# Kernel tuning notes

Hardware: AMD Instinct MI355X
Metric: run time of the kernel (lower is better)

## Reference

```python
import jax, jax.numpy as jnp
import numpy as np

NEG_INF = -1e30


def setup_inputs() -> dict:
    key = jax.random.key(0)
    kx, km, kq, kk, kv, ko = jax.random.split(key, 6)
    B, D, L = 2, 1024, 2048
    H, DK = 16, 64
    x = jax.random.normal(kx, (B, D, L), dtype=jnp.float32)
    mask = (jax.random.uniform(km, (B, L)) < 0.9).astype(jnp.float32)
    # per-head projection weights, stacked: (H, D, DK); output proj (D, H*DK)==(D, D)
    sq = 1.0 / np.sqrt(D)
    Wq = jax.random.normal(kq, (H, D, DK), dtype=jnp.float32) * sq
    Wk = jax.random.normal(kk, (H, D, DK), dtype=jnp.float32) * sq
    Wv = jax.random.normal(kv, (H, D, DK), dtype=jnp.float32) * sq
    Wo = jax.random.normal(ko, (D, H * DK), dtype=jnp.float32) * sq
    return {"x": x, "mask": mask, "Wq": Wq, "Wk": Wk, "Wv": Wv, "Wo": Wo}


def reference(x, mask, Wq, Wk, Wv, Wo):
    # x: (B, D, L); original transposes to (B, L, D)
    B, D, L = x.shape
    H, _, DK = Wq.shape
    xt = jnp.transpose(x, (0, 2, 1))  # (B, L, D)
    q = jnp.einsum('bld,hdk->bhlk', xt, Wq)
    k = jnp.einsum('bld,hdk->bhlk', xt, Wk)
    v = jnp.einsum('bld,hdk->bhlk', xt, Wv)
    scores = jnp.einsum('bhlk,bhmk->bhlm', q, k) * (1.0 / np.sqrt(DK))
    # masked log-softmax over keys (hmask), squad-style: mask*logit + (1-mask)*-1e30
    hmask = mask[:, None, None, :]  # (B,1,1,Lk)
    masked = hmask * scores + (1.0 - hmask) * NEG_INF
    logp = jax.nn.log_softmax(masked, axis=-1)
    # second softmax over the log-probs, then multiplicative vmask on query dim
    p = jax.nn.softmax(logp, axis=-1) * mask[:, None, :, None]
    heads = jnp.einsum('bhlm,bhmk->bhlk', p, v)  # (B,H,L,DK)
    head = jnp.transpose(heads, (0, 2, 1, 3)).reshape(B, L, H * DK)
    out = jnp.einsum('ble,de->bld', head, Wo)  # matmul(head, Wo) with Wo (D, H*DK)... 
    # NOTE: torch.matmul(head, Wo) treats Wo as (H*DK_in, D_out) only if square; here
    # Wo is (D, H*DK) with D == H*DK, and torch contracts head's last dim with Wo's FIRST dim:
    out = head @ Wo  # (B, L, H*DK) @ (D, H*DK) requires D==H*DK; contracts dim 0 of Wo
    return jnp.transpose(out, (0, 2, 1))  # (B, D, L)


if __name__ == "__main__":
    print(reference(**setup_inputs()).shape)
```

## Files before the change

### kernel.cpp

```cpp
#include <hip/hip_runtime.h>
#include <hip/hip_bf16.h>

typedef unsigned short u16;
typedef unsigned int u32;
typedef unsigned long long u64;
typedef short s8v __attribute__((ext_vector_type(8)));
typedef short s4v __attribute__((ext_vector_type(4)));
typedef __bf16 bfv8 __attribute__((ext_vector_type(8)));
typedef float f4 __attribute__((ext_vector_type(4)));

static constexpr int B = 2, D = 1024, L = 2048, H = 16, DK = 64, E = 1024;
static constexpr float QSCALE = 0.125f * 1.44269504088896340736f;
static constexpr float SMB = -16.0f;
static constexpr float MASKB = -12000.0f;

#define DEV __device__ __forceinline__

DEV u16 f2bf(float f) {
  unsigned int u = __float_as_uint(f);
  u += 0x7FFFu + ((u >> 16) & 1u);
  return (u16)(u >> 16);
}
DEV float fexp2(float x) { return __builtin_amdgcn_exp2f(x); }
DEV u32 pkbf(float a, float b) {
  __hip_bfloat162 h = __float22bfloat162_rn(float2{a, b});
  u32 r;
  __builtin_memcpy(&r, &h, 4);
  return r;
}
DEV bfv8 cat8(s4v a, s4v b) {
  s8v r;
#pragma unroll
  for (int i = 0; i < 4; ++i) {
    r[i] = a[i];
    r[i + 4] = b[i];
  }
  return __builtin_bit_cast(bfv8, r);
}
DEV int kperm(int kk) {
  return (kk & 96) | (((kk >> 2) & 3) << 3) | (((kk >> 4) & 1) << 2) |
         (kk & 3);
}

#define GLD_LDS16(gp, lp)                                                     \
  __builtin_amdgcn_global_load_lds(                                           \
      (const __attribute__((address_space(1))) void*)(gp),                    \
      (__attribute__((address_space(3))) void*)(lp), 16, 0, 0)

__global__ __launch_bounds__(256) void k_prep(
    const float* __restrict__ x, const float* __restrict__ Wq,
    const float* __restrict__ Wk, const float* __restrict__ Wv,
    const float* __restrict__ Wo, u16* __restrict__ xt, u16* __restrict__ Wt,
    u16* __restrict__ WoT) {
  __shared__ u16 t[64][67];
  const int tid = threadIdx.x;
  const int g = blockIdx.x;
  const float* src;
  u16* dst;
  int sld, dld;
  if (g < 1024) {
    const int b = g >> 9, dt = (g >> 5) & 15, lt = g & 31;
    src = x + ((size_t)b * D + dt * 64) * L + lt * 64;
    sld = L;
    dst = xt + ((size_t)b * L + lt * 64) * D + dt * 64;
    dld = D;
  } else if (g < 1792) {
    const int u = g - 1024;
    const int w = u >> 8, h = (u >> 4) & 15, dt = u & 15;
    const float* Ws = (w == 0) ? Wq : ((w == 1) ? Wk : Wv);
    src = Ws + ((size_t)h * D + dt * 64) * DK;
    sld = DK;
    dst = Wt + ((size_t)(w * H + h) * DK) * D + dt * 64;
    dld = D;
  } else {
    const int v = g - 1792;
    const int et = v >> 4, dt = v & 15;
    src = Wo + ((size_t)et * 64) * D + dt * 64;
    sld = D;
    dst = WoT + ((size_t)dt * 64) * E + et * 64;
    dld = E;
  }
  const int r = tid >> 2, c16 = (tid & 3) * 16;
#pragma unroll
  for (int j = 0; j < 16; j += 4) {
    const f4 v4 = *(const f4*)(src + (size_t)r * sld + c16 + j);
    t[r][c16 + j]     = f2bf(v4[0]);
    t[r][c16 + j + 1] = f2bf(v4[1]);
    t[r][c16 + j + 2] = f2bf(v4[2]);
    t[r][c16 + j + 3] = f2bf(v4[3]);
  }
  __syncthreads();
  s8v o0, o1;
#pragma unroll
  for (int i = 0; i < 8; ++i) {
    o0[i] = (short)t[c16 + i][r];
    o1[i] = (short)t[c16 + 8 + i][r];
  }
  *(s8v*)(dst + (size_t)r * dld + c16)     = o0;
  *(s8v*)(dst + (size_t)r * dld + c16 + 8) = o1;
}

template <int AR>
DEV void gemm_tile(const u16* __restrict__ A, const u16* __restrict__ Bt,
                   int arow0, int brow0, u16* As, u16* Bs,
                   f4 (&acc)[AR / 32][4]) {
  const int tid = threadIdx.x;
  const int wid = tid >> 6, lane = tid & 63;
  const int q = lane >> 4, ln = lane & 15;
  const int wr = wid >> 1, wc = wid & 1;
  const int lrow = lane >> 3;
  const int lc = (lane & 7) ^ lrow;
  const int f0 = (q ^ (ln & 7)) * 8;
  const int f1 = ((q + 4) ^ (ln & 7)) * 8;
  constexpr int MT = AR / 32;

  for (int k0 = 0; k0 < 1024; k0 += 64) {
    __syncthreads();
#pragma unroll
    for (int j = 0; j < AR / 32; ++j) {
      const int rb = wid * (AR / 4) + j * 8;
      GLD_LDS16(A + (size_t)(arow0 + rb + lrow) * 1024 + k0 + lc * 8,
                As + rb * 64);
    }
#pragma unroll
    for (int j = 0; j < 4; ++j) {
      const int rb = wid * 32 + j * 8;
      GLD_LDS16(Bt + (size_t)(brow0 + rb + lrow) * 1024 + k0 + lc * 8,
                Bs + rb * 64);
    }
    __syncthreads();
#pragma unroll
    for (int ks = 0; ks < 2; ++ks) {
      const int fc = ks ? f1 : f0;
      bfv8 af[MT], bf[4];
#pragma unroll
      for (int mt = 0; mt < MT; ++mt)
        af[mt] = *(const bfv8*)(As + (wr * (AR / 2) + mt * 16 + ln) * 64 + fc);
#pragma unroll
      for (int nt = 0; nt < 4; ++nt)
        bf[nt] = *(const bfv8*)(Bs + (wc * 64 + nt * 16 + ln) * 64 + fc);
#pragma unroll
      for (int mt = 0; mt < MT; ++mt)
#pragma unroll
        for (int nt = 0; nt < 4; ++nt)
          acc[mt][nt] = __builtin_amdgcn_mfma_f32_16x16x32_bf16(
              af[mt], bf[nt], acc[mt][nt], 0, 0, 0);
    }
  }
}

__global__ __launch_bounds__(256, 3) void k_qkvg(
    const u16* __restrict__ xt, const u16* __restrict__ Wt,
    u16* __restrict__ Q, u16* __restrict__ K, u16* __restrict__ Vt) {
  __shared__ u16 As[128 * 64];
  __shared__ u16 Bs[128 * 64];
  const int bm = blockIdx.x, bn = blockIdx.y;
  f4 acc[4][4];
#pragma unroll
  for (int mt = 0; mt < 4; ++mt)
#pragma unroll
    for (int nt = 0; nt < 4; ++nt) acc[mt][nt] = (f4){0.f, 0.f, 0.f, 0.f};
  gemm_tile<128>(xt, Wt, bm * 128, bn * 128, As, Bs, acc);

  const int tid = threadIdx.x, wid = tid >> 6, lane = tid & 63;
  const int q = lane >> 4, ln = lane & 15;
  const int wr = wid >> 1, wc = wid & 1;
  const int h2 = bn * 2 + wc;
  const int wsel = h2 >> 4, h = h2 & 15;
  const int b = bm >> 4;
  const int lbase = (bm & 15) * 128 + wr * 64;
  if (wsel == 0) {
    u16* dst = Q + (size_t)(b * H + h) * L * DK;
#pragma unroll
    for (int mt = 0; mt < 4; ++mt)
#pragma unroll
      for (int nt = 0; nt < 4; ++nt)
#pragma unroll
        for (int r = 0; r < 4; ++r)
          dst[(size_t)(lbase + mt * 16 + q * 4 + r) * DK + nt * 16 + ln] =
              f2bf(acc[mt][nt][r] * QSCALE);
  } else if (wsel == 1) {
    u16* dst = K + (size_t)(b * H + h) * L * DK;
#pragma unroll
    for (int mt = 0; mt < 4; ++mt)
#pragma unroll
      for (int nt = 0; nt < 4; ++nt)
#pragma unroll
        for (int r = 0; r < 4; ++r)
          dst[(size_t)(lbase + mt * 16 + q * 4 + r) * DK + nt * 16 + ln] =
              f2bf(acc[mt][nt][r]);
  } else {
    u16* dst = Vt + (size_t)(b * H + h) * DK * L;
#pragma unroll
    for (int mt = 0; mt < 4; ++mt)
#pragma unroll
      for (int nt = 0; nt < 4; ++nt) {
        const u64 pk = (u64)pkbf(acc[mt][nt][0], acc[mt][nt][1]) |
                       ((u64)pkbf(acc[mt][nt][2], acc[mt][nt][3]) << 32);
        *(u64*)(dst + (size_t)(nt * 16 + ln) * L + lbase + mt * 16 + q * 4) =
            pk;
      }
  }
}

__global__ __launch_bounds__(512, 4) void k_attn(
    const u16* __restrict__ Q, const u16* __restrict__ K,
    const u16* __restrict__ Vt, const float* __restrict__ mask,
    u16* __restrict__ Hd) {
  __shared__ u16 kt[2][128 * 64];
  __shared__ u16 vt[2][2][64 * 64];
  __shared__ __align__(16) float mb[L];
  const int h = blockIdx.x, lt = blockIdx.y, b = blockIdx.z;
  const int tid = threadIdx.x;
  const int w = tid >> 6, lane = tid & 63, q = lane >> 4, ln = lane & 15;
  const int wq = w >> 1, wk = w & 1;
  for (int i = tid; i < L; i += 512)
    mb[i] = (mask[(size_t)b * L + i] != 0.0f) ? SMB : MASKB;

  const int bh = b * H + h;
  const u16* Qp = Q + (size_t)bh * L * DK;
  const u16* Kp = K + (size_t)bh * L * DK;
  const u16* Vp = Vt + (size_t)bh * DK * L;
  const int lq = lt * 128 + wq * 32;

  bfv8 qf[2][2];
#pragma unroll
  for (int mt = 0; mt < 2; ++mt) {
    qf[mt][0] = *(const bfv8*)(Qp + (size_t)(lq + mt * 16 + ln) * DK + q * 8);
    qf[mt][1] =
        *(const bfv8*)(Qp + (size_t)(lq + mt * 16 + ln) * DK + 32 + q * 8);
  }

  const int lrow = lane >> 3;
  const int lc = (lane & 7) ^ lrow;
  const int c0 = (q ^ (ln & 7)) * 8;
  const int c1 = ((q + 4) ^ (ln & 7)) * 8;
  int kpr[2];
#pragma unroll
  for (int j = 0; j < 2; ++j) kpr[j] = kperm(w * 16 + j * 8 + lrow);

  auto stage = [&](int m0, int bufi) {
#pragma unroll
    for (int j = 0; j < 2; ++j) {
      GLD_LDS16(Kp + (size_t)(m0 + kpr[j]) * DK + lc * 8,
                &kt[bufi][(w * 16 + j * 8) * 64]);
    }
    const int fr = w * 8 + lrow;
#pragma unroll
    for (int kh = 0; kh < 2; ++kh) {
      GLD_LDS16(Vp + (size_t)fr * L + m0 + kh * 64 + lc * 8,
                &vt[bufi][kh][(w * 8) * 64]);
    }
  };

  union {
    f4 v;
    float f[4];
  } ot[2][4];
#pragma unroll
  for (int mt = 0; mt < 2; ++mt)
#pragma unroll
    for (int dt = 0; dt < 4; ++dt) ot[mt][dt].v = (f4){0.f, 0.f, 0.f, 0.f};
  float lp[2] = {0.f, 0.f};

  stage(0, 0);
  for (int it = 0; it < L / 128; ++it) {
    const int m0 = it * 128;
    __syncthreads();
    if (it + 1 < L / 128) stage(m0 + 128, (it + 1) & 1);
    const int cur = it & 1;
    const u16* ktc = &kt[cur][0];
    const u16* vtc = &vt[cur][wk][0];

    s4v pbe[2];
    bfv8 pbx[2][2];
#pragma unroll
    for (int nt = 0; nt < 4; ++nt) {
      const int krow = wk * 64 + nt * 16 + ln;
      const bfv8 kf0 = *(const bfv8*)(ktc + krow * 64 + c0);
      const bfv8 kf1 = *(const bfv8*)(ktc + krow * 64 + c1);
      const f4 mbv = *(const f4*)(mb + m0 + wk * 64 + (nt >> 1) * 32 +
                                  (nt & 1) * 4 + q * 8);
#pragma unroll
      for (int mt = 0; mt < 2; ++mt) {
        f4 a = mbv;
        __builtin_amdgcn_s_setprio(1);
        a = __builtin_amdgcn_mfma_f32_16x16x32_bf16(kf0, qf[mt][0], a, 0, 0,
                                                    0);
        a = __builtin_amdgcn_mfma_f32_16x16x32_bf16(kf1, qf[mt][1], a, 0, 0,
                                                    0);
        __builtin_amdgcn_s_setprio(0);
        const float p0 = fexp2(a[0]);
        const float p1 = fexp2(a[1]);
        const float p2 = fexp2(a[2]);
        const float p3 = fexp2(a[3]);
        lp[mt] += (p0 + p1) + (p2 + p3);
        const u64 pk = (u64)pkbf(p0, p1) | ((u64)pkbf(p2, p3) << 32);
        const s4v pc = __builtin_bit_cast(s4v, pk);
        if (nt & 1)
          pbx[mt][nt >> 1] = cat8(pbe[mt], pc);
        else
          pbe[mt] = pc;
      }
    }
    __builtin_amdgcn_s_setprio(1);
#pragma unroll
    for (int g = 0; g < 2; ++g) {
#pragma unroll
      for (int dt = 0; dt < 4; ++dt) {
        const int vrow = dt * 16 + ln;
        const bfv8 av =
            *(const bfv8*)(vtc + vrow * 64 + (((g * 4 + q) ^ (ln & 7)) * 8));
#pragma unroll
        for (int mt = 0; mt < 2; ++mt)
          ot[mt][dt].v = __builtin_amdgcn_mfma_f32_16x16x32_bf16(
              av, pbx[mt][g], ot[mt][dt].v, 0, 0, 0);
      }
    }
    __builtin_amdgcn_s_setprio(0);
  }
#pragma unroll
  for (int mt = 0; mt < 2; ++mt) {
    lp[mt] += __shfl_xor(lp[mt], 16);
    lp[mt] += __shfl_xor(lp[mt], 32);
  }
  __syncthreads();
  float* sOt = (float*)&kt[0][0];
  float* sLp = (float*)&vt[0][0][0];
  if (wk) {
#pragma unroll
    for (int mt = 0; mt < 2; ++mt) {
#pragma unroll
      for (int dt = 0; dt < 4; ++dt)
        *(f4*)(sOt + ((((wq * 2 + mt) * 4 + dt) * 64) + lane) * 4) =
            ot[mt][dt].v;
      sLp[(wq * 2 + mt) * 64 + lane] = lp[mt];
    }
  }
  __syncthreads();
  if (!wk) {
#pragma unroll
    for (int mt = 0; mt < 2; ++mt) {
#pragma unroll
      for (int dt = 0; dt < 4; ++dt)
        ot[mt][dt].v +=
            *(const f4*)(sOt + ((((wq * 2 + mt) * 4 + dt) * 64) + lane) * 4);
      lp[mt] += sLp[(wq * 2 + mt) * 64 + lane];
      const float linv =
          (mb[lq + mt * 16 + ln] > -100.0f) ? (1.0f / lp[mt]) : 0.0f;
#pragma unroll
      for (int dt = 0; dt < 4; ++dt) {
        const u64 pk =
            (u64)pkbf(ot[mt][dt].f[0] * linv, ot[mt][dt].f[1] * linv) |
            ((u64)pkbf(ot[mt][dt].f[2] * linv, ot[mt][dt].f[3] * linv) << 32);
        *(u64*)(Hd + (size_t)(b * L + lq + mt * 16 + ln) * E + h * DK +
                dt * 16 + q * 4) = pk;
      }
    }
  }
}

__global__ __launch_bounds__(256, 2) void k_projg(const u16* __restrict__ WoT,
                                                  const u16* __restrict__ Hd,
                                                  float* __restrict__ out) {
  __shared__ u16 As[64 * 64];
  __shared__ u16 Bs[128 * 64];
  const int bm = blockIdx.x, bn = blockIdx.y;
  f4 acc[2][4];
#pragma unroll
  for (int mt = 0; mt < 2; ++mt)
#pragma unroll
    for (int nt = 0; nt < 4; ++nt) acc[mt][nt] = (f4){0.f, 0.f, 0.f, 0.f};
  gemm_tile<64>(WoT, Hd, bm * 64, bn * 128, As, Bs, acc);

  const int tid = threadIdx.x, wid = tid >> 6, lane = tid & 63;
  const int q = lane >> 4, ln = lane & 15;
  const int wr = wid >> 1, wc = wid & 1;
#pragma unroll
  for (int mt = 0; mt < 2; ++mt)
#pragma unroll
    for (int nt = 0; nt < 4; ++nt)
#pragma unroll
      for (int r = 0; r < 4; ++r) {
        const int d = bm * 64 + wr * 32 + mt * 16 + q * 4 + r;
        const int n = bn * 128 + wc * 64 + nt * 16 + ln;
        const int bb = n >> 11, l = n & 2047;
        out[((size_t)(bb * D + d)) * L + l] = acc[mt][nt][r];
      }
}

extern "C" void kernel_launch(void* const* d_in, const int* in_sizes, int n_in,
                              void* d_out, int out_size, void* d_ws,
                              size_t ws_size, hipStream_t stream) {
  const float* x    = (const float*)d_in[0];
  const float* mask = (const float*)d_in[1];
  const float* Wq   = (const float*)d_in[2];
  const float* Wk   = (const float*)d_in[3];
  const float* Wv   = (const float*)d_in[4];
  const float* Wo   = (const float*)d_in[5];
  u16* ws = (u16*)d_ws;
  u16* Qws  = ws;
  u16* Kws  = ws + 4194304;
  u16* Vtws = ws + 8388608;
  u16* WoTw = ws + 12582912;
  u16* Wtws = ws + 13631488;
  u16* xtws = ws + 16777216;
  u16* Hdws = ws + 16777216;

  k_prep<<<2048, 256, 0, stream>>>(x, Wq, Wk, Wv, Wo, xtws, Wtws, WoTw);
  k_qkvg<<<dim3(32, 24), 256, 0, stream>>>(xtws, Wtws, Qws, Kws, Vtws);
  k_attn<<<dim3(16, 16, 2), 512, 0, stream>>>(Qws, Kws, Vtws, mask, Hdws);
  k_projg<<<dim3(16, 32), 256, 0, stream>>>(WoTw, Hdws, (float*)d_out);
}
```

Baseline: 174.0 us.

## Remap block indices per XCD for L2 locality and shrink projection tiles

All three GEMM/attention launches become 1D grids. Block IDs are remapped so that blocks scheduled on the same XCD (round-robin by blockIdx mod 8) share A/B tiles or the same batch-head, which should improve per-XCD L2 reuse. The output projection also moves to 64x64 tiles with a higher occupancy bound, giving 1024 blocks instead of 512. Smaller tiles lower arithmetic intensity per block and add redundant operand loads.

```diff
diff --git a/kernel.cpp b/kernel.cpp
--- a/kernel.cpp
+++ b/kernel.cpp
@@ -100,10 +100,10 @@
   *(s8v*)(dst + (size_t)r * dld + c16 + 8) = o1;
 }
 
-template <int AR>
+template <int AR, int BR>
 DEV void gemm_tile(const u16* __restrict__ A, const u16* __restrict__ Bt,
                    int arow0, int brow0, u16* As, u16* Bs,
-                   f4 (&acc)[AR / 32][4]) {
+                   f4 (&acc)[AR / 32][BR / 32]) {
   const int tid = threadIdx.x;
   const int wid = tid >> 6, lane = tid & 63;
   const int q = lane >> 4, ln = lane & 15;
@@ -112,7 +112,7 @@
   const int lc = (lane & 7) ^ lrow;
   const int f0 = (q ^ (ln & 7)) * 8;
   const int f1 = ((q + 4) ^ (ln & 7)) * 8;
-  constexpr int MT = AR / 32;
+  constexpr int MT = AR / 32, NT = BR / 32;
 
   for (int k0 = 0; k0 < 1024; k0 += 64) {
     __syncthreads();
@@ -123,8 +123,8 @@
                 As + rb * 64);
     }
 #pragma unroll
-    for (int j = 0; j < 4; ++j) {
-      const int rb = wid * 32 + j * 8;
+    for (int j = 0; j < BR / 32; ++j) {
+      const int rb = wid * (BR / 4) + j * 8;
       GLD_LDS16(Bt + (size_t)(brow0 + rb + lrow) * 1024 + k0 + lc * 8,
                 Bs + rb * 64);
     }
@@ -132,17 +132,17 @@
 #pragma unroll
     for (int ks = 0; ks < 2; ++ks) {
       const int fc = ks ? f1 : f0;
-      bfv8 af[MT], bf[4];
+      bfv8 af[MT], bf[NT];
 #pragma unroll
       for (int mt = 0; mt < MT; ++mt)
         af[mt] = *(const bfv8*)(As + (wr * (AR / 2) + mt * 16 + ln) * 64 + fc);
 #pragma unroll
-      for (int nt = 0; nt < 4; ++nt)
-        bf[nt] = *(const bfv8*)(Bs + (wc * 64 + nt * 16 + ln) * 64 + fc);
+      for (int nt = 0; nt < NT; ++nt)
+        bf[nt] = *(const bfv8*)(Bs + (wc * (BR / 2) + nt * 16 + ln) * 64 + fc);
 #pragma unroll
       for (int mt = 0; mt < MT; ++mt)
 #pragma unroll
-        for (int nt = 0; nt < 4; ++nt)
+        for (int nt = 0; nt < NT; ++nt)
           acc[mt][nt] = __builtin_amdgcn_mfma_f32_16x16x32_bf16(
               af[mt], bf[nt], acc[mt][nt], 0, 0, 0);
     }
@@ -154,13 +154,16 @@
     u16* __restrict__ Q, u16* __restrict__ K, u16* __restrict__ Vt) {
   __shared__ u16 As[128 * 64];
   __shared__ u16 Bs[128 * 64];
-  const int bm = blockIdx.x, bn = blockIdx.y;
+  const int orig = blockIdx.x;
+  const int xcd = orig & 7, kk = orig >> 3;
+  const int bm = (xcd >> 1) * 8 + (kk & 7);
+  const int bn = (xcd & 1) * 12 + (kk >> 3);
   f4 acc[4][4];
 #pragma unroll
   for (int mt = 0; mt < 4; ++mt)
 #pragma unroll
     for (int nt = 0; nt < 4; ++nt) acc[mt][nt] = (f4){0.f, 0.f, 0.f, 0.f};
-  gemm_tile<128>(xt, Wt, bm * 128, bn * 128, As, Bs, acc);
+  gemm_tile<128, 128>(xt, Wt, bm * 128, bn * 128, As, Bs, acc);
 
   const int tid = threadIdx.x, wid = tid >> 6, lane = tid & 63;
   const int q = lane >> 4, ln = lane & 15;
@@ -210,14 +213,17 @@
   __shared__ u16 kt[2][128 * 64];
   __shared__ u16 vt[2][2][64 * 64];
   __shared__ __align__(16) float mb[L];
-  const int h = blockIdx.x, lt = blockIdx.y, b = blockIdx.z;
+  const int orig = blockIdx.x;
+  const int xcd = orig & 7, kk2 = orig >> 3;
+  const int bh = xcd * 4 + (kk2 >> 4);
+  const int lt = kk2 & 15;
+  const int b = bh >> 4, h = bh & 15;
   const int tid = threadIdx.x;
   const int w = tid >> 6, lane = tid & 63, q = lane >> 4, ln = lane & 15;
   const int wq = w >> 1, wk = w & 1;
   for (int i = tid; i < L; i += 512)
     mb[i] = (mask[(size_t)b * L + i] != 0.0f) ? SMB : MASKB;
 
-  const int bh = b * H + h;
   const u16* Qp = Q + (size_t)bh * L * DK;
   const u16* Kp = K + (size_t)bh * L * DK;
   const u16* Vp = Vt + (size_t)bh * DK * L;
@@ -360,18 +366,21 @@
   }
 }
 
-__global__ __launch_bounds__(256, 2) void k_projg(const u16* __restrict__ WoT,
+__global__ __launch_bounds__(256, 4) void k_projg(const u16* __restrict__ WoT,
                                                   const u16* __restrict__ Hd,
                                                   float* __restrict__ out) {
   __shared__ u16 As[64 * 64];
-  __shared__ u16 Bs[128 * 64];
-  const int bm = blockIdx.x, bn = blockIdx.y;
-  f4 acc[2][4];
+  __shared__ u16 Bs[64 * 64];
+  const int orig = blockIdx.x;
+  const int xcd = orig & 7, kk = orig >> 3;
+  const int bm = kk & 15;
+  const int bn = xcd * 8 + (kk >> 4);
+  f4 acc[2][2];
 #pragma unroll
   for (int mt = 0; mt < 2; ++mt)
 #pragma unroll
-    for (int nt = 0; nt < 4; ++nt) acc[mt][nt] = (f4){0.f, 0.f, 0.f, 0.f};
-  gemm_tile<64>(WoT, Hd, bm * 64, bn * 128, As, Bs, acc);
+    for (int nt = 0; nt < 2; ++nt) acc[mt][nt] = (f4){0.f, 0.f, 0.f, 0.f};
+  gemm_tile<64, 64>(WoT, Hd, bm * 64, bn * 64, As, Bs, acc);
 
   const int tid = threadIdx.x, wid = tid >> 6, lane = tid & 63;
   const int q = lane >> 4, ln = lane & 15;
@@ -379,11 +388,11 @@
 #pragma unroll
   for (int mt = 0; mt < 2; ++mt)
 #pragma unroll
-    for (int nt = 0; nt < 4; ++nt)
+    for (int nt = 0; nt < 2; ++nt)
 #pragma unroll
       for (int r = 0; r < 4; ++r) {
         const int d = bm * 64 + wr * 32 + mt * 16 + q * 4 + r;
-        const int n = bn * 128 + wc * 64 + nt * 16 + ln;
+        const int n = bn * 64 + wc * 32 + nt * 16 + ln;
         const int bb = n >> 11, l = n & 2047;
         out[((size_t)(bb * D + d)) * L + l] = acc[mt][nt][r];
       }
@@ -408,7 +417,7 @@
   u16* Hdws = ws + 16777216;
 
   k_prep<<<2048, 256, 0, stream>>>(x, Wq, Wk, Wv, Wo, xtws, Wtws, WoTw);
-  k_qkvg<<<dim3(32, 24), 256, 0, stream>>>(xtws, Wtws, Qws, Kws, Vtws);
-  k_attn<<<dim3(16, 16, 2), 512, 0, stream>>>(Qws, Kws, Vtws, mask, Hdws);
-  k_projg<<<dim3(16, 32), 256, 0, stream>>>(WoTw, Hdws, (float*)d_out);
-}
+  k_qkvg<<<768, 256, 0, stream>>>(xtws, Wtws, Qws, Kws, Vtws);
+  k_attn<<<512, 512, 0, stream>>>(Qws, Kws, Vtws, mask, Hdws);
+  k_projg<<<1024, 256, 0, stream>>>(WoTw, Hdws, (float*)d_out);
+}
```

After: 168.4 us. 3.2% less time.
